# Performance work log

Measured on AMD Instinct MI355X. Metric: run time of the kernel, lower is better.

## Reference

```python
import jax, jax.numpy as jnp
import numpy as np

B, N, L, C, K = 2, 8192, 8192, 128, 8
RADIUS = 0.4

def _gather(t, idx):
    # t: [B,L,D], idx: [B,N,K] -> [B,N,K,D]
    b, n, k = idx.shape
    return jnp.take_along_axis(t, idx.reshape(b, n * k)[:, :, None], axis=1).reshape(b, n, k, t.shape[-1])

def _ln(x, g, b):
    m = x.mean(-1, keepdims=True)
    v = x.var(-1, keepdims=True)
    return (x - m) * jax.lax.rsqrt(v + 1e-5) * g + b

def setup_inputs() -> dict:
    key = jax.random.key(0)
    ks = jax.random.split(key, 16)
    F = 4 * C
    def w(k, i, o):
        return jax.random.normal(k, (i, o), jnp.float32) / np.sqrt(i).astype(np.float32)
    return {
        "q_xyz": jax.random.uniform(ks[0], (B, N, 3), jnp.float32),
        "q_feat": jax.random.normal(ks[1], (B, N, C), jnp.float32),
        "kv_xyz": jax.random.uniform(ks[2], (B, L, 3), jnp.float32),
        "kv_feat": jax.random.normal(ks[3], (B, L, C), jnp.float32),
        "kv_pad": jnp.zeros((B, L), bool),
        "pos_w1": w(ks[4], 3, C), "pos_b1": jnp.zeros((C,), jnp.float32),
        "pos_w2": w(ks[5], C, C), "pos_b2": jnp.zeros((C,), jnp.float32),
        "attn_w": w(ks[6], C, C), "attn_b": jnp.zeros((C,), jnp.float32),
        "lin_w": w(ks[7], C, C),
        "lin_src_w": w(ks[8], C, C),
        "lin_dst_w": w(ks[9], C, C),
        "ln1_g": jnp.ones((C,), jnp.float32), "ln1_b": jnp.zeros((C,), jnp.float32),
        "ffn_w1": w(ks[10], C, F), "ffn_b1": jnp.zeros((F,), jnp.float32),
        "ffn_w2": w(ks[11], F, C), "ffn_b2": jnp.zeros((C,), jnp.float32),
        "ln2_g": jnp.ones((C,), jnp.float32), "ln2_b": jnp.zeros((C,), jnp.float32),
    }

def reference(q_xyz, q_feat, kv_xyz, kv_feat, kv_pad,
              pos_w1, pos_b1, pos_w2, pos_b2, attn_w, attn_b,
              lin_w, lin_src_w, lin_dst_w, ln1_g, ln1_b,
              ffn_w1, ffn_b1, ffn_w2, ffn_b2, ln2_g, ln2_b):
    # --- radius graph: up to K nearest kv points within RADIUS per query ---
    d2 = jnp.sum((q_xyz[:, :, None, :] - kv_xyz[:, None, :, :]) ** 2, -1)  # [B,N,L]
    ok = (d2 <= RADIUS ** 2) & (~kv_pad)[:, None, :]
    neg_d2, idx = jax.lax.top_k(jnp.where(ok, -d2, -jnp.inf), K)  # [B,N,K]
    ev = jnp.isfinite(neg_d2)  # edge-valid mask [B,N,K]

    # --- PointTransformerConv (vector attention, per-edge) ---
    pos_j = _gather(kv_xyz, idx)                           # [B,N,K,3]
    rel = q_xyz[:, :, None, :] - pos_j                     # pos_i - pos_j
    # pos_nn: MLP([3,C,C], plain_last=False) => ReLU after each Linear
    delta = jax.nn.relu(jax.nn.relu(rel @ pos_w1 + pos_b1) @ pos_w2 + pos_b2)  # [B,N,K,C]
    a_src = _gather(kv_feat @ lin_src_w, idx)              # [B,N,K,C]
    a_dst = q_feat @ lin_dst_w                             # [B,N,C]
    x_j = _gather(kv_feat @ lin_w, idx)                    # [B,N,K,C]
    # attn_nn: MLP([C,C], plain_last=False) => Linear + ReLU
    alpha = jax.nn.relu((a_dst[:, :, None, :] - a_src + delta) @ attn_w + attn_b)
    # segment softmax over the K neighbors (invalid edges masked out)
    scores = jnp.where(ev[..., None], alpha, -jnp.inf)
    mx = jnp.max(scores, axis=2, keepdims=True)
    mx = jnp.where(jnp.isfinite(mx), mx, 0.0)
    e = jnp.where(ev[..., None], jnp.exp(scores - mx), 0.0)
    attn = e / jnp.maximum(e.sum(2, keepdims=True), 1e-12)
    agg = jnp.sum(attn * (x_j + delta), axis=2)            # [B,N,C]

    # --- residual + LN + FFN + LN (dropout = identity at eval) ---
    out = _ln(q_feat + agg, ln1_g, ln1_b)
    h = jax.nn.gelu(out @ ffn_w1 + ffn_b1, approximate=False) @ ffn_w2 + ffn_b2
    return _ln(out + h, ln2_g, ln2_b)
```

## Files before the change

### kernel.cpp

```cpp
#include <hip/hip_runtime.h>
#include <math.h>

#define NB 2
#define NQ 8192
#define NL 8192
#define NC 128
#define NKN 8
#define NF 512
#define MQ (NB*NQ)

typedef __attribute__((ext_vector_type(8))) short bf16x8;
typedef __attribute__((ext_vector_type(4))) float f32x4;

__device__ __forceinline__ unsigned short f2bf_u(float f){
    unsigned u = __float_as_uint(f);
    return (unsigned short)((u + 0x7FFFu + ((u>>16)&1u)) >> 16);
}
__device__ __forceinline__ float bf2f(unsigned short s){
    return __uint_as_float(((unsigned)s) << 16);
}


__device__ __forceinline__ int cell_coord(float x) {
    int c = (int)(x * 16.0f);
    return min(15, max(0, c));
}

__global__ __launch_bounds__(256) void grid_count_kernel(
    const float* __restrict__ kxyz, const unsigned char* __restrict__ pad,
    int* __restrict__ cnt)
{
    int t = blockIdx.x*256 + threadIdx.x;
    if (pad[t]) return;
    int bat = t >> 13;
    float x = kxyz[t*3+0], y = kxyz[t*3+1], z = kxyz[t*3+2];
    int cell = (cell_coord(z)*16 + cell_coord(y))*16 + cell_coord(x);
    atomicAdd(&cnt[bat*4096 + cell], 1);
}

__global__ __launch_bounds__(1024) void grid_scan_kernel(
    const int* __restrict__ cnt, int* __restrict__ cs)
{
    __shared__ int wsum[17];
    int t = threadIdx.x;
    int v[8]; int s = 0;
    #pragma unroll
    for (int k = 0; k < 8; ++k) { v[k] = s; s += cnt[t*8 + k]; }
    int lane = t & 63, w = t >> 6;
    int inc = s;
    #pragma unroll
    for (int d = 1; d < 64; d <<= 1) {
        int o = __shfl_up(inc, d);
        if (lane >= d) inc += o;
    }
    if (lane == 63) wsum[w] = inc;
    __syncthreads();
    if (t == 0) {
        int a = 0;
        for (int i = 0; i < 16; ++i) { int x = wsum[i]; wsum[i] = a; a += x; }
        wsum[16] = a;
    }
    __syncthreads();
    int base = wsum[w] + (inc - s);
    #pragma unroll
    for (int k = 0; k < 8; ++k) cs[t*8 + k] = base + v[k];
    if (t == 1023) cs[8192] = wsum[16];
}

__global__ __launch_bounds__(256) void grid_scatter_kernel(
    const float* __restrict__ kxyz, const unsigned char* __restrict__ pad,
    const int* __restrict__ cs, int* __restrict__ fill, float4* __restrict__ ro)
{
    int t = blockIdx.x*256 + threadIdx.x;
    if (pad[t]) return;
    int bat = t >> 13, i = t & 8191;
    float x = kxyz[t*3+0], y = kxyz[t*3+1], z = kxyz[t*3+2];
    int cell = bat*4096 + (cell_coord(z)*16 + cell_coord(y))*16 + cell_coord(x);
    int pos = cs[cell] + atomicAdd(&fill[cell], 1);
    ro[pos] = make_float4(x, y, z, __int_as_float(i));
}

__device__ __forceinline__ void insert8(float cd, int id, float dk[8], int ik[8]) {
    if (cd < dk[7]) {
        dk[7] = cd; ik[7] = id;
        #pragma unroll
        for (int r = 6; r >= 0; --r) {
            bool sw = dk[r+1] < dk[r];
            float td = dk[r]; int ti = ik[r];
            dk[r]   = sw ? dk[r+1] : dk[r];
            ik[r]   = sw ? ik[r+1] : ik[r];
            dk[r+1] = sw ? td : dk[r+1];
            ik[r+1] = sw ? ti : ik[r+1];
        }
    }
}

template<int W>
__device__ __forceinline__ void scan_block(int l, int cx, int cy, int cz,
    float qx, float qy, float qz, const int* __restrict__ CS,
    const float4* __restrict__ RO, float dk[8], int ik[8])
{
    const int D = 2*W + 1;
    int xs = max(0, cx - W), xe = min(15, cx + W);
    int nx = xe - xs + 1;
    for (int r = l; r < D*D; r += 8) {
        int dz = r / D - W, dy = r % D - W;
        int zz = cz + dz, yy = cy + dy;
        if ((unsigned)zz > 15u || (unsigned)yy > 15u) continue;
        int c0 = (zz*16 + yy)*16 + xs;
        int s = CS[c0], e = CS[c0 + nx];
        for (int p = s; p < e; ++p) {
            float4 v = RO[p];
            float dx = qx - v.x, dyv = qy - v.y, dzv = qz - v.z;
            float cd = dx*dx + dyv*dyv + dzv*dzv;
            insert8(cd, __float_as_int(v.w), dk, ik);
        }
    }
}

__device__ __forceinline__ void merge8(float dk[8], int ik[8]) {
    #pragma unroll
    for (int m = 1; m <= 4; m <<= 1) {
        float od[8]; int oi[8];
        #pragma unroll
        for (int r = 0; r < 8; ++r) {
            od[r] = __shfl_xor(dk[r], m);
            oi[r] = __shfl_xor(ik[r], m);
        }
        float nd[8]; int ni[8];
        #pragma unroll
        for (int r = 0; r < 8; ++r) {
            bool take = od[7-r] < dk[r];
            nd[r] = take ? od[7-r] : dk[r];
            ni[r] = take ? oi[7-r] : ik[r];
        }
        #pragma unroll
        for (int st = 4; st >= 1; st >>= 1) {
            #pragma unroll
            for (int r = 0; r < 8; ++r) {
                if ((r & st) == 0 && (r | st) < 8) {
                    int b = r | st;
                    bool sw = nd[b] < nd[r];
                    float td = nd[r]; int ti = ni[r];
                    nd[r] = sw ? nd[b] : nd[r];
                    ni[r] = sw ? ni[b] : ni[r];
                    nd[b] = sw ? td : nd[b];
                    ni[b] = sw ? ti : ni[b];
                }
            }
        }
        #pragma unroll
        for (int r = 0; r < 8; ++r) { dk[r] = nd[r]; ik[r] = ni[r]; }
    }
}

__global__ __launch_bounds__(256) void radius_grid_query_kernel(
    const float* __restrict__ qxyz, const int* __restrict__ cellstart,
    const float4* __restrict__ reorder, int* __restrict__ idxout)
{
    const int tid  = threadIdx.x;
    const int l    = tid & 7;
    const int qloc = tid >> 3;
    const int gq   = blockIdx.x*32 + qloc;
    const int bat  = gq >> 13;
    const float qx = qxyz[gq*3+0], qy = qxyz[gq*3+1], qz = qxyz[gq*3+2];
    const int cx = cell_coord(qx), cy = cell_coord(qy), cz = cell_coord(qz);
    const int* CS = cellstart + bat*4096;
    const float R2  = (float)(0.4*0.4);
    const float R2P = __uint_as_float(__float_as_uint(R2) + 1u);

    float dk[8]; int ik[8];
    #pragma unroll
    for (int r = 0; r < 8; ++r) { dk[r] = R2P; ik[r] = -1; }

    scan_block<2>(l, cx, cy, cz, qx, qy, qz, CS, reorder, dk, ik);
    merge8(dk, ik);
    bool done = dk[7] <= 0.015625f;

    if (!done) {
        #pragma unroll
        for (int r = 0; r < 8; ++r) { dk[r] = R2P; ik[r] = -1; }
        scan_block<4>(l, cx, cy, cz, qx, qy, qz, CS, reorder, dk, ik);
        merge8(dk, ik);
        done = dk[7] <= 0.0625f;
    }
    if (!done) {
        #pragma unroll
        for (int r = 0; r < 8; ++r) { dk[r] = R2P; ik[r] = -1; }
        scan_block<16>(l, cx, cy, cz, qx, qy, qz, CS, reorder, dk, ik);
        merge8(dk, ik);
    }

    if (l == 0) {
        int o[8];
        #pragma unroll
        for (int r = 0; r < 8; ++r) o[r] = (dk[r] <= R2) ? ik[r] : -1;
        int4 a = {o[0], o[1], o[2], o[3]};
        int4 b = {o[4], o[5], o[6], o[7]};
        *(int4*)&idxout[(size_t)gq*8 + 0] = a;
        *(int4*)&idxout[(size_t)gq*8 + 4] = b;
    }
}

__global__ __launch_bounds__(256) void prep_all_kernel(
    const float* __restrict__ posw2, const float* __restrict__ attnw,
    const float* __restrict__ lin_w, const float* __restrict__ lin_src_w,
    const float* __restrict__ lin_dst_w,
    const float* __restrict__ ffn_w1, const float* __restrict__ ffn_w2,
    unsigned short* __restrict__ imgb, int* __restrict__ zero_p)
{
    int t = blockIdx.x*256 + threadIdx.x;
    if (t < 16384) {
        int k = t >> 7, n = t & 127;
        imgb[(k >> 5)*4096 + n*32 + (k & 31)] = f2bf_u(posw2[t]);
    } else if (t < 32768) {
        int u = t - 16384;
        int k = u >> 7, n = u & 127;
        imgb[16384 + (k >> 5)*4096 + n*32 + (k & 31)] = f2bf_u(attnw[u]);
    } else if (t < 65536) {
        int u = t - 32768;
        int k = u >> 8, n = u & 255;
        float v = (n < 128) ? lin_w[k*128 + n] : lin_src_w[k*128 + (n-128)];
        imgb[32768 + ((k >> 5)*256 + n)*32 + (k & 31)] = f2bf_u(v);
    } else if (t < 81920) {
        int u = t - 65536;
        int k = u >> 7, n = u & 127;
        imgb[65536 + ((k >> 5)*128 + n)*32 + (k & 31)] = f2bf_u(lin_dst_w[u]);
    } else if (t < 147456) {
        int u = t - 81920;
        int k = u >> 9, n = u & 511;
        imgb[81920 + ((k >> 5)*512 + n)*32 + (k & 31)] = f2bf_u(ffn_w1[u]);
    } else if (t < 212992) {
        int u = t - 147456;
        int k = u >> 7, n = u & 127;
        imgb[147456 + ((k >> 5)*128 + n)*32 + (k & 31)] = f2bf_u(ffn_w2[u]);
    } else {
        zero_p[t - 212992] = 0;
    }
}

__global__ __launch_bounds__(256) void lin3_kernel(
    const float* __restrict__ kv_feat, const float* __restrict__ q_feat,
    const unsigned short* __restrict__ wvs, const unsigned short* __restrict__ wd,
    unsigned short* __restrict__ vs, float* __restrict__ adst)
{
    __shared__ unsigned short sA[64*32];
    __shared__ unsigned short sB[128*32];
    const int tid = threadIdx.x;
    const int w = tid >> 6, lane = tid & 63, l15 = lane & 15, quad = lane >> 4;
    const int row0 = blockIdx.x*64;
    const int y = blockIdx.y;
    const float* A = (y == 2) ? q_feat : kv_feat;
    const unsigned short* Bimg = (y == 2) ? wd : wvs;
    const int BNd = (y == 2) ? 128 : 256;
    const int col0 = (y == 2) ? 0 : y*128;

    f32x4 acc[8];
    #pragma unroll
    for (int t=0;t<8;t++){ acc[t][0]=0.f; acc[t][1]=0.f; acc[t][2]=0.f; acc[t][3]=0.f; }

    for (int kc = 0; kc < 4; ++kc) {
        __syncthreads();
        #pragma unroll
        for (int it = 0; it < 2; ++it) {
            int ix = it*256 + tid;
            int r = ix >> 3, kq = ix & 7;
            float4 a4 = *(const float4*)&A[(size_t)(row0+r)*NC + kc*32 + kq*4];
            ushort4 pk = { f2bf_u(a4.x), f2bf_u(a4.y), f2bf_u(a4.z), f2bf_u(a4.w) };
            *(ushort4*)&sA[r*32 + kq*4] = pk;
        }
        const int4* bsrc = (const int4*)(Bimg + ((size_t)kc*BNd + col0)*32);
        #pragma unroll
        for (int it = 0; it < 2; ++it) {
            int o = it*256 + tid;
            ((int4*)sB)[o] = bsrc[o];
        }
        __syncthreads();
        bf16x8 af = *(const bf16x8*)&sA[(w*16 + l15)*32 + quad*8];
        #pragma unroll
        for (int t = 0; t < 8; ++t) {
            bf16x8 bf = *(const bf16x8*)&sB[(16*t + l15)*32 + quad*8];
            acc[t] = __builtin_amdgcn_mfma_f32_16x16x32_bf16(af, bf, acc[t], 0, 0, 0);
        }
    }

    const int rowb = row0 + w*16 + quad*4;
    #pragma unroll
    for (int t = 0; t < 8; ++t) {
        int col = col0 + 16*t + l15;
        #pragma unroll
        for (int r = 0; r < 4; ++r) {
            if (y == 2) adst[(size_t)(rowb+r)*NC + col] = acc[t][r];
            else        vs[(size_t)(rowb+r)*256 + col] = f2bf_u(acc[t][r]);
        }
    }
}

__device__ inline float gelu_exact(float x) {
    return 0.5f*x*(1.0f + erff(x*0.7071067811865476f));
}

__global__ __launch_bounds__(256, 4) void ffn_fused_kernel(
    const float* __restrict__ in1,
    const unsigned short* __restrict__ wf1, const unsigned short* __restrict__ wf2,
    const float* __restrict__ b1v, const float* __restrict__ b2v,
    const float* __restrict__ g, const float* __restrict__ bb,
    float* __restrict__ out)
{
    __shared__ unsigned short sH[4*16*136];
    __shared__ float4 sS[16];
    __shared__ float4 sQ[16];
    const int tid = threadIdx.x;
    const int w = tid >> 6, lane = tid & 63, l15 = lane & 15, quad = lane >> 4;
    const int row0 = blockIdx.x*16;

    bf16x8 af[4];
    {
        const float* arow = in1 + (size_t)(row0 + l15)*NC;
        #pragma unroll
        for (int kk = 0; kk < 4; ++kk) {
            float4 a0 = *(const float4*)&arow[kk*32 + quad*8];
            float4 a1 = *(const float4*)&arow[kk*32 + quad*8 + 4];
            bf16x8 v;
            v[0]=(short)f2bf_u(a0.x); v[1]=(short)f2bf_u(a0.y);
            v[2]=(short)f2bf_u(a0.z); v[3]=(short)f2bf_u(a0.w);
            v[4]=(short)f2bf_u(a1.x); v[5]=(short)f2bf_u(a1.y);
            v[6]=(short)f2bf_u(a1.z); v[7]=(short)f2bf_u(a1.w);
            af[kk] = v;
        }
    }

    f32x4 acc1[8];
    #pragma unroll
    for (int t=0;t<8;t++){ acc1[t][0]=0.f; acc1[t][1]=0.f; acc1[t][2]=0.f; acc1[t][3]=0.f; }
    #pragma unroll
    for (int kk=0;kk<4;kk++){
        #pragma unroll
        for (int t=0;t<8;t++){
            int n = w*128 + 16*t + l15;
            bf16x8 bf = *(const bf16x8*)&wf1[((size_t)kk*512 + n)*32 + quad*8];
            acc1[t] = __builtin_amdgcn_mfma_f32_16x16x32_bf16(af[kk], bf, acc1[t], 0, 0, 0);
        }
    }

    {
        unsigned short* Hw = sH + w*(16*136);
        #pragma unroll
        for (int t=0;t<8;t++){
            float bv = b1v[w*128 + 16*t + l15];
            #pragma unroll
            for (int r=0;r<4;r++){
                float x = gelu_exact(acc1[t][r] + bv);
                Hw[(quad*4+r)*136 + 16*t + l15] = f2bf_u(x);
            }
        }
    }
    __syncthreads();

    f32x4 acc2[2];
    #pragma unroll
    for (int tt=0;tt<2;tt++){ acc2[tt][0]=0.f; acc2[tt][1]=0.f; acc2[tt][2]=0.f; acc2[tt][3]=0.f; }
    #pragma unroll
    for (int kkg=0;kkg<16;kkg++){
        const unsigned short* Ht = sH + (kkg>>2)*(16*136);
        bf16x8 a2 = *(const bf16x8*)&Ht[l15*136 + (kkg&3)*32 + quad*8];
        #pragma unroll
        for (int tt=0;tt<2;tt++){
            int col = (2*w+tt)*16 + l15;
            bf16x8 bf = *(const bf16x8*)&wf2[((size_t)kkg*128 + col)*32 + quad*8];
            acc2[tt] = __builtin_amdgcn_mfma_f32_16x16x32_bf16(a2, bf, acc2[tt], 0, 0, 0);
        }
    }

    float xv[2][4];
    float S0=0.f,S1=0.f,S2=0.f,S3=0.f;
    float Q0=0.f,Q1=0.f,Q2=0.f,Q3=0.f;
    #pragma unroll
    for (int tt=0;tt<2;tt++){
        int col = (2*w+tt)*16 + l15;
        float bv = b2v[col];
        #pragma unroll
        for (int r=0;r<4;r++){
            int row = row0 + quad*4 + r;
            float x = acc2[tt][r] + bv + in1[(size_t)row*NC + col];
            xv[tt][r] = x;
            if (r==0){ S0+=x; Q0+=x*x; } else if (r==1){ S1+=x; Q1+=x*x; }
            else if (r==2){ S2+=x; Q2+=x*x; } else { S3+=x; Q3+=x*x; }
        }
    }
    #pragma unroll
    for (int m=1;m<=8;m<<=1){
        S0 += __shfl_xor(S0,m); S1 += __shfl_xor(S1,m);
        S2 += __shfl_xor(S2,m); S3 += __shfl_xor(S3,m);
        Q0 += __shfl_xor(Q0,m); Q1 += __shfl_xor(Q1,m);
        Q2 += __shfl_xor(Q2,m); Q3 += __shfl_xor(Q3,m);
    }
    if (l15 == 0){
        sS[w*4 + quad] = make_float4(S0,S1,S2,S3);
        sQ[w*4 + quad] = make_float4(Q0,Q1,Q2,Q3);
    }
    __syncthreads();

    float4 St = sS[quad]; float4 Qt = sQ[quad];
    {
        float4 a = sS[4+quad],  b = sS[8+quad],  c = sS[12+quad];
        St.x += a.x+b.x+c.x; St.y += a.y+b.y+c.y; St.z += a.z+b.z+c.z; St.w += a.w+b.w+c.w;
        float4 d = sQ[4+quad], e = sQ[8+quad],  f = sQ[12+quad];
        Qt.x += d.x+e.x+f.x; Qt.y += d.y+e.y+f.y; Qt.z += d.z+e.z+f.z; Qt.w += d.w+e.w+f.w;
    }
    float mean[4], rstd[4];
    {
        float sv[4] = {St.x, St.y, St.z, St.w};
        float qv[4] = {Qt.x, Qt.y, Qt.z, Qt.w};
        #pragma unroll
        for (int r=0;r<4;r++){
            float m_ = sv[r]*(1.f/128.f);
            float v_ = qv[r]*(1.f/128.f) - m_*m_;
            mean[r] = m_;
            rstd[r] = rsqrtf(v_ + 1e-5f);
        }
    }
    #pragma unroll
    for (int tt=0;tt<2;tt++){
        int col = (2*w+tt)*16 + l15;
        float gv = g[col], bv = bb[col];
        #pragma unroll
        for (int r=0;r<4;r++){
            int row = row0 + quad*4 + r;
            out[(size_t)row*NC + col] = (xv[tt][r]-mean[r])*rstd[r]*gv + bv;
        }
    }
}

__global__ __launch_bounds__(256) void attn_mfma_kernel(
    const float* __restrict__ qxyz, const float* __restrict__ qfeat,
    const float* __restrict__ kxyz,
    const float* __restrict__ posw1, const float* __restrict__ posb1,
    const float* __restrict__ posb2, const float* __restrict__ attnb,
    const float* __restrict__ ln1g, const float* __restrict__ ln1b,
    const unsigned short* __restrict__ wimg1, const unsigned short* __restrict__ wimg2,
    const int* __restrict__ idx, const unsigned short* __restrict__ vs,
    const float* __restrict__ adst, float* __restrict__ out1)
{
    __shared__ unsigned short s_w[16384];
    __shared__ unsigned short s_V[4*16*136];
    __shared__ unsigned short s_T[4*16*136];
    __shared__ float s_w1[384];
    __shared__ float s_b1[128], s_b2[128], s_ab[128], s_g[128], s_bb[128];
    __shared__ int   s_j[64];

    const int tid  = threadIdx.x;
    const int w    = tid >> 6;
    const int lane = tid & 63;
    const int l15  = lane & 15;
    const int quad = lane >> 4;
    const int qbase = blockIdx.x*8 + w*2;
    const int bat  = (blockIdx.x*8) >> 13;

    if (tid < 128) {
        s_b1[tid] = posb1[tid]; s_b2[tid] = posb2[tid];
        s_ab[tid] = attnb[tid]; s_g[tid] = ln1g[tid]; s_bb[tid] = ln1b[tid];
    } else {
        int i = tid - 128;
        s_w1[i] = posw1[i]; s_w1[128+i] = posw1[128+i]; s_w1[256+i] = posw1[256+i];
    }
    if (tid < 64) s_j[tid] = idx[(size_t)blockIdx.x*64 + tid];
    #pragma unroll
    for (int r = 0; r < 8; ++r)
        ((int4*)s_w)[r*256 + tid] = ((const int4*)wimg1)[r*256 + tid];
    __syncthreads();

    #pragma unroll
    for (int i = 0; i < 4; ++i) {
        int ix = lane + i*64;
        int el = ix >> 4, c16 = ix & 15;
        int j = s_j[w*16 + el];
        int jc = j < 0 ? 0 : j;
        const int4* rp = (const int4*)(vs + ((size_t)(bat*NL + jc))*256);
        int dst = (w*16 + el)*136 + c16*8;
        *(int4*)&s_V[dst] = rp[c16];
        *(int4*)&s_T[dst] = rp[16 + c16];
    }

    bf16x8 h1f[4];
    {
        int e  = w*16 + l15;
        int qh = qbase + (l15 >> 3);
        int j  = s_j[e];
        int jc = j < 0 ? 0 : j;
        const float* kp = kxyz + ((size_t)(bat*NL + jc))*3;
        float rx = qxyz[qh*3+0]-kp[0], ry = qxyz[qh*3+1]-kp[1], rz = qxyz[qh*3+2]-kp[2];
        #pragma unroll
        for (int kk=0;kk<4;kk++){
            #pragma unroll
            for (int jj=0;jj<8;jj++){
                int c = kk*32 + quad*8 + jj;
                float h = s_b1[c] + rx*s_w1[c] + ry*s_w1[128+c] + rz*s_w1[256+c];
                h = fmaxf(h, 0.f);
                h1f[kk][jj] = (short)f2bf_u(h);
            }
        }
    }

    f32x4 acc[8];
    #pragma unroll
    for (int t=0;t<8;t++){ acc[t][0]=0.f; acc[t][1]=0.f; acc[t][2]=0.f; acc[t][3]=0.f; }
    #pragma unroll
    for (int kk=0;kk<4;kk++){
        #pragma unroll
        for (int t=0;t<8;t++){
            bf16x8 wf = *(const bf16x8*)&s_w[kk*4096 + (16*t + l15)*32 + quad*8];
            acc[t] = __builtin_amdgcn_mfma_f32_16x16x32_bf16(h1f[kk], wf, acc[t], 0, 0, 0);
        }
    }

    f32x4 dreg[8];
    #pragma unroll
    for (int t=0;t<8;t++){
        float b2v = s_b2[16*t + l15];
        #pragma unroll
        for (int r=0;r<4;r++) dreg[t][r] = fmaxf(acc[t][r] + b2v, 0.f);
    }

    int jr[4]; bool val[4];
    #pragma unroll
    for (int r=0;r<4;r++){
        int j = s_j[w*16 + quad*4 + r];
        val[r] = (j >= 0); jr[r] = j < 0 ? 0 : j;
    }
    const int qt = qbase + (quad >> 1);
    float ad[8];
    #pragma unroll
    for (int t=0;t<8;t++) ad[t] = adst[(size_t)qt*NC + 16*t + l15];

    __syncthreads();

    #pragma unroll
    for (int r = 0; r < 8; ++r)
        ((int4*)s_w)[r*256 + tid] = ((const int4*)wimg2)[r*256 + tid];

    {
        unsigned short* st = s_T + w*16*136;
        #pragma unroll
        for (int t=0;t<8;t++){
            #pragma unroll
            for (int r=0;r<4;r++){
                int o = (quad*4 + r)*136 + 16*t + l15;
                float sv = bf2f(st[o]);
                st[o] = f2bf_u(ad[t] - sv + dreg[t][r]);
            }
        }
    }
    __syncthreads();

    f32x4 acc2[8];
    #pragma unroll
    for (int t=0;t<8;t++){ acc2[t][0]=0.f; acc2[t][1]=0.f; acc2[t][2]=0.f; acc2[t][3]=0.f; }
    {
        const unsigned short* st = s_T + w*16*136;
        #pragma unroll
        for (int kk=0;kk<4;kk++){
            bf16x8 tf = *(const bf16x8*)&st[l15*136 + kk*32 + quad*8];
            #pragma unroll
            for (int t=0;t<8;t++){
                bf16x8 wf = *(const bf16x8*)&s_w[kk*4096 + (16*t + l15)*32 + quad*8];
                acc2[t] = __builtin_amdgcn_mfma_f32_16x16x32_bf16(tf, wf, acc2[t], 0, 0, 0);
            }
        }
    }

    float ex[8][4]; float dnm[8];
    #pragma unroll
    for (int t=0;t<8;t++){
        float ab = s_ab[16*t + l15];
        float s0 = val[0] ? fmaxf(acc2[t][0] + ab, 0.f) : -INFINITY;
        float s1 = val[1] ? fmaxf(acc2[t][1] + ab, 0.f) : -INFINITY;
        float s2 = val[2] ? fmaxf(acc2[t][2] + ab, 0.f) : -INFINITY;
        float s3 = val[3] ? fmaxf(acc2[t][3] + ab, 0.f) : -INFINITY;
        float mx = fmaxf(fmaxf(s0,s1), fmaxf(s2,s3));
        mx = fmaxf(mx, __shfl_xor(mx, 16));
        if (mx < -1e37f) mx = 0.f;
        ex[t][0] = __expf(s0 - mx);
        ex[t][1] = __expf(s1 - mx);
        ex[t][2] = __expf(s2 - mx);
        ex[t][3] = __expf(s3 - mx);
        float sm = ex[t][0]+ex[t][1]+ex[t][2]+ex[t][3];
        sm += __shfl_xor(sm, 16);
        dnm[t] = fmaxf(sm, 1e-12f);
    }

    float part[8];
    #pragma unroll
    for (int t=0;t<8;t++){
        float p = 0.f;
        #pragma unroll
        for (int r=0;r<4;r++){
            float vv = bf2f(s_V[(w*16 + quad*4 + r)*136 + 16*t + l15]);
            p += ex[t][r] * (vv + dreg[t][r]);
        }
        p += __shfl_xor(p, 16);
        part[t] = p / dnm[t];
    }

    float xln[8];
    float S = 0.f;
    #pragma unroll
    for (int t=0;t<8;t++){
        xln[t] = qfeat[(size_t)qt*NC + 16*t + l15] + part[t];
        S += xln[t];
    }
    #pragma unroll
    for (int m=1;m<=8;m<<=1) S += __shfl_xor(S, m);
    float mean = S * (1.f/128.f);
    float V = 0.f;
    #pragma unroll
    for (int t=0;t<8;t++){ float d = xln[t]-mean; V += d*d; }
    #pragma unroll
    for (int m=1;m<=8;m<<=1) V += __shfl_xor(V, m);
    float rstd = rsqrtf(V*(1.f/128.f) + 1e-5f);

    if ((quad & 1) == 0){
        #pragma unroll
        for (int t=0;t<8;t++){
            int c = 16*t + l15;
            out1[(size_t)qt*NC + c] = (xln[t]-mean)*rstd*s_g[c] + s_bb[c];
        }
    }
}

extern "C" void kernel_launch(void* const* d_in, const int* in_sizes, int n_in,
                              void* d_out, int out_size, void* d_ws, size_t ws_size,
                              hipStream_t stream)
{
    (void)in_sizes; (void)n_in; (void)out_size; (void)ws_size;
    const float* q_xyz   = (const float*)d_in[0];
    const float* q_feat  = (const float*)d_in[1];
    const float* kv_xyz  = (const float*)d_in[2];
    const float* kv_feat = (const float*)d_in[3];
    const unsigned char* kv_pad = (const unsigned char*)d_in[4];
    const float* pos_w1  = (const float*)d_in[5];
    const float* pos_b1  = (const float*)d_in[6];
    const float* pos_w2  = (const float*)d_in[7];
    const float* pos_b2  = (const float*)d_in[8];
    const float* attn_w  = (const float*)d_in[9];
    const float* attn_b  = (const float*)d_in[10];
    const float* lin_w   = (const float*)d_in[11];
    const float* lin_src_w = (const float*)d_in[12];
    const float* lin_dst_w = (const float*)d_in[13];
    const float* ln1_g   = (const float*)d_in[14];
    const float* ln1_b   = (const float*)d_in[15];
    const float* ffn_w1  = (const float*)d_in[16];
    const float* ffn_b1  = (const float*)d_in[17];
    const float* ffn_w2  = (const float*)d_in[18];
    const float* ffn_b2  = (const float*)d_in[19];
    const float* ln2_g   = (const float*)d_in[20];
    const float* ln2_b   = (const float*)d_in[21];

    float* ws    = (float*)d_ws;
    int*   idx   = (int*)d_ws;
    unsigned short* vs = (unsigned short*)(ws + 131072);
    float* adst  = ws + 131072 + 2*2097152;
    float* out1  = adst + 2097152;
    float* Hreg  = out1 + 2097152;

    float4* reorder  = (float4*)Hreg;
    int* cellcnt   = (int*)(reorder + 16384);
    int* cellfill  = cellcnt + 8192;
    int* cellstart = cellfill + 8192;

    unsigned short* imgb  = (unsigned short*)((char*)Hreg + (1u << 20));
    unsigned short* wimg1 = imgb;
    unsigned short* wimg2 = imgb + 16384;
    unsigned short* wvs   = imgb + 32768;
    unsigned short* wd    = imgb + 65536;
    unsigned short* wf1   = imgb + 81920;
    unsigned short* wf2   = imgb + 147456;

    prep_all_kernel<<<dim3(896), dim3(256), 0, stream>>>(
        pos_w2, attn_w, lin_w, lin_src_w, lin_dst_w, ffn_w1, ffn_w2, imgb, cellcnt);

    grid_count_kernel<<<dim3(64), dim3(256), 0, stream>>>(kv_xyz, kv_pad, cellcnt);
    grid_scan_kernel<<<dim3(1), dim3(1024), 0, stream>>>(cellcnt, cellstart);
    grid_scatter_kernel<<<dim3(64), dim3(256), 0, stream>>>(kv_xyz, kv_pad, cellstart, cellfill, reorder);
    radius_grid_query_kernel<<<dim3(MQ/32), dim3(256), 0, stream>>>(q_xyz, cellstart, reorder, idx);

    lin3_kernel<<<dim3(MQ/64, 3), dim3(256), 0, stream>>>(kv_feat, q_feat, wvs, wd, vs, adst);

    attn_mfma_kernel<<<dim3(MQ/8), dim3(256), 0, stream>>>(
        q_xyz, q_feat, kv_xyz,
        pos_w1, pos_b1, pos_b2, attn_b, ln1_g, ln1_b,
        wimg1, wimg2, idx, vs, adst, out1);

    ffn_fused_kernel<<<dim3(MQ/16), dim3(256), 0, stream>>>(
        out1, wf1, wf2, ffn_b1, ffn_b2, ln2_g, ln2_b, (float*)d_out);
}
```

Baseline: 219.7 us.

## Read attention MLP weights from global instead of LDS to raise occupancy

Drops the 32KB shared-memory staging of the two bf16 weight images in the attention kernel. MFMA B-fragments are now loaded straight from global memory, relying on the L1/L2 caches. Removing the staging also removes two block-wide barriers, since the remaining LDS buffers are only used within each wave. It adds a launch-bounds occupancy hint and fuses the softmax and aggregation loops to lower register pressure. The risk is higher global/L2 traffic and latency on weight fetches inside the MFMA loops.

Measured after the change: 223.6 us. No clear change (+1.8%).

```diff
diff --git a/kernel.cpp b/kernel.cpp
--- a/kernel.cpp
+++ b/kernel.cpp
@@ -432,7 +432,7 @@
     }
 }
 
-__global__ __launch_bounds__(256) void attn_mfma_kernel(
+__global__ __launch_bounds__(256, 4) void attn_mfma_kernel(
     const float* __restrict__ qxyz, const float* __restrict__ qfeat,
     const float* __restrict__ kxyz,
     const float* __restrict__ posw1, const float* __restrict__ posb1,
@@ -442,7 +442,6 @@
     const int* __restrict__ idx, const unsigned short* __restrict__ vs,
     const float* __restrict__ adst, float* __restrict__ out1)
 {
-    __shared__ unsigned short s_w[16384];
     __shared__ unsigned short s_V[4*16*136];
     __shared__ unsigned short s_T[4*16*136];
     __shared__ float s_w1[384];
@@ -465,9 +464,6 @@
         s_w1[i] = posw1[i]; s_w1[128+i] = posw1[128+i]; s_w1[256+i] = posw1[256+i];
     }
     if (tid < 64) s_j[tid] = idx[(size_t)blockIdx.x*64 + tid];
-    #pragma unroll
-    for (int r = 0; r < 8; ++r)
-        ((int4*)s_w)[r*256 + tid] = ((const int4*)wimg1)[r*256 + tid];
     __syncthreads();
 
     #pragma unroll
@@ -509,7 +505,7 @@
     for (int kk=0;kk<4;kk++){
         #pragma unroll
         for (int t=0;t<8;t++){
-            bf16x8 wf = *(const bf16x8*)&s_w[kk*4096 + (16*t + l15)*32 + quad*8];
+            bf16x8 wf = *(const bf16x8*)&wimg1[kk*4096 + (16*t + l15)*32 + quad*8];
             acc[t] = __builtin_amdgcn_mfma_f32_16x16x32_bf16(h1f[kk], wf, acc[t], 0, 0, 0);
         }
     }
@@ -522,22 +518,16 @@
         for (int r=0;r<4;r++) dreg[t][r] = fmaxf(acc[t][r] + b2v, 0.f);
     }
 
-    int jr[4]; bool val[4];
+    bool val[4];
     #pragma unroll
     for (int r=0;r<4;r++){
         int j = s_j[w*16 + quad*4 + r];
-        val[r] = (j >= 0); jr[r] = j < 0 ? 0 : j;
+        val[r] = (j >= 0);
     }
     const int qt = qbase + (quad >> 1);
     float ad[8];
     #pragma unroll
     for (int t=0;t<8;t++) ad[t] = adst[(size_t)qt*NC + 16*t + l15];
-
-    __syncthreads();
-
-    #pragma unroll
-    for (int r = 0; r < 8; ++r)
-        ((int4*)s_w)[r*256 + tid] = ((const int4*)wimg2)[r*256 + tid];
 
     {
         unsigned short* st = s_T + w*16*136;
@@ -551,7 +541,6 @@
             }
         }
     }
-    __syncthreads();
 
     f32x4 acc2[8];
     #pragma unroll
@@ -563,13 +552,13 @@
             bf16x8 tf = *(const bf16x8*)&st[l15*136 + kk*32 + quad*8];
             #pragma unroll
             for (int t=0;t<8;t++){
-                bf16x8 wf = *(const bf16x8*)&s_w[kk*4096 + (16*t + l15)*32 + quad*8];
+                bf16x8 wf = *(const bf16x8*)&wimg2[kk*4096 + (16*t + l15)*32 + quad*8];
                 acc2[t] = __builtin_amdgcn_mfma_f32_16x16x32_bf16(tf, wf, acc2[t], 0, 0, 0);
             }
         }
     }
 
-    float ex[8][4]; float dnm[8];
+    float part[8];
     #pragma unroll
     for (int t=0;t<8;t++){
         float ab = s_ab[16*t + l15];
@@ -580,26 +569,20 @@
         float mx = fmaxf(fmaxf(s0,s1), fmaxf(s2,s3));
         mx = fmaxf(mx, __shfl_xor(mx, 16));
         if (mx < -1e37f) mx = 0.f;
-        ex[t][0] = __expf(s0 - mx);
-        ex[t][1] = __expf(s1 - mx);
-        ex[t][2] = __expf(s2 - mx);
-        ex[t][3] = __expf(s3 - mx);
-        float sm = ex[t][0]+ex[t][1]+ex[t][2]+ex[t][3];
+        float e0 = __expf(s0 - mx);
+        float e1 = __expf(s1 - mx);
+        float e2 = __expf(s2 - mx);
+        float e3 = __expf(s3 - mx);
+        float sm = e0+e1+e2+e3;
         sm += __shfl_xor(sm, 16);
-        dnm[t] = fmaxf(sm, 1e-12f);
-    }
-
-    float part[8];
-    #pragma unroll
-    for (int t=0;t<8;t++){
+        float dnm = fmaxf(sm, 1e-12f);
         float p = 0.f;
-        #pragma unroll
-        for (int r=0;r<4;r++){
-            float vv = bf2f(s_V[(w*16 + quad*4 + r)*136 + 16*t + l15]);
-            p += ex[t][r] * (vv + dreg[t][r]);
-        }
+        p += e0 * (bf2f(s_V[(w*16 + quad*4 + 0)*136 + 16*t + l15]) + dreg[t][0]);
+        p += e1 * (bf2f(s_V[(w*16 + quad*4 + 1)*136 + 16*t + l15]) + dreg[t][1]);
+        p += e2 * (bf2f(s_V[(w*16 + quad*4 + 2)*136 + 16*t + l15]) + dreg[t][2]);
+        p += e3 * (bf2f(s_V[(w*16 + quad*4 + 3)*136 + 16*t + l15]) + dreg[t][3]);
         p += __shfl_xor(p, 16);
-        part[t] = p / dnm[t];
+        part[t] = p / dnm;
     }
 
     float xln[8];
```

## Double rows per block in FFN and attention kernels to amortize weight loads

Applied to the files above, without the earlier changes.

The FFN kernel now handles 32 rows per block instead of 16. Each block computes two 16-row tiles, so every weight fragment loaded from global memory feeds two MFMAs. The attention kernel grows to 512 threads covering 16 queries, so the shared weight images are staged once for twice the work. The cost is more registers and shared memory per block, which may lower occupancy, and the grids have half as many blocks.

Measured after the change: 216.6 us. No clear change (-1.4%).

```diff
diff --git a/kernel.cpp b/kernel.cpp
--- a/kernel.cpp
+++ b/kernel.cpp
@@ -300,139 +300,169 @@
     return 0.5f*x*(1.0f + erff(x*0.7071067811865476f));
 }
 
-__global__ __launch_bounds__(256, 4) void ffn_fused_kernel(
+__global__ __launch_bounds__(256) void ffn_fused_kernel(
     const float* __restrict__ in1,
     const unsigned short* __restrict__ wf1, const unsigned short* __restrict__ wf2,
     const float* __restrict__ b1v, const float* __restrict__ b2v,
     const float* __restrict__ g, const float* __restrict__ bb,
     float* __restrict__ out)
 {
-    __shared__ unsigned short sH[4*16*136];
-    __shared__ float4 sS[16];
-    __shared__ float4 sQ[16];
+    __shared__ unsigned short sH[8*16*136];
+    __shared__ float4 sS[2][16];
+    __shared__ float4 sQ[2][16];
     const int tid = threadIdx.x;
     const int w = tid >> 6, lane = tid & 63, l15 = lane & 15, quad = lane >> 4;
-    const int row0 = blockIdx.x*16;
-
-    bf16x8 af[4];
+    const int row0 = blockIdx.x*32;
+
+    bf16x8 af0[4], af1[4];
     {
-        const float* arow = in1 + (size_t)(row0 + l15)*NC;
+        const float* arow0 = in1 + (size_t)(row0 + l15)*NC;
+        const float* arow1 = in1 + (size_t)(row0 + 16 + l15)*NC;
         #pragma unroll
         for (int kk = 0; kk < 4; ++kk) {
-            float4 a0 = *(const float4*)&arow[kk*32 + quad*8];
-            float4 a1 = *(const float4*)&arow[kk*32 + quad*8 + 4];
+            float4 a0 = *(const float4*)&arow0[kk*32 + quad*8];
+            float4 a1 = *(const float4*)&arow0[kk*32 + quad*8 + 4];
             bf16x8 v;
             v[0]=(short)f2bf_u(a0.x); v[1]=(short)f2bf_u(a0.y);
             v[2]=(short)f2bf_u(a0.z); v[3]=(short)f2bf_u(a0.w);
             v[4]=(short)f2bf_u(a1.x); v[5]=(short)f2bf_u(a1.y);
             v[6]=(short)f2bf_u(a1.z); v[7]=(short)f2bf_u(a1.w);
-            af[kk] = v;
-        }
-    }
-
-    f32x4 acc1[8];
-    #pragma unroll
-    for (int t=0;t<8;t++){ acc1[t][0]=0.f; acc1[t][1]=0.f; acc1[t][2]=0.f; acc1[t][3]=0.f; }
+            af0[kk] = v;
+            float4 b0 = *(const float4*)&arow1[kk*32 + quad*8];
+            float4 b1 = *(const float4*)&arow1[kk*32 + quad*8 + 4];
+            bf16x8 u;
+            u[0]=(short)f2bf_u(b0.x); u[1]=(short)f2bf_u(b0.y);
+            u[2]=(short)f2bf_u(b0.z); u[3]=(short)f2bf_u(b0.w);
+            u[4]=(short)f2bf_u(b1.x); u[5]=(short)f2bf_u(b1.y);
+            u[6]=(short)f2bf_u(b1.z); u[7]=(short)f2bf_u(b1.w);
+            af1[kk] = u;
+        }
+    }
+
+    f32x4 acc1a[8], acc1b[8];
+    #pragma unroll
+    for (int t=0;t<8;t++){
+        acc1a[t][0]=0.f; acc1a[t][1]=0.f; acc1a[t][2]=0.f; acc1a[t][3]=0.f;
+        acc1b[t][0]=0.f; acc1b[t][1]=0.f; acc1b[t][2]=0.f; acc1b[t][3]=0.f;
+    }
     #pragma unroll
     for (int kk=0;kk<4;kk++){
         #pragma unroll
         for (int t=0;t<8;t++){
             int n = w*128 + 16*t + l15;
             bf16x8 bf = *(const bf16x8*)&wf1[((size_t)kk*512 + n)*32 + quad*8];
-            acc1[t] = __builtin_amdgcn_mfma_f32_16x16x32_bf16(af[kk], bf, acc1[t], 0, 0, 0);
+            acc1a[t] = __builtin_amdgcn_mfma_f32_16x16x32_bf16(af0[kk], bf, acc1a[t], 0, 0, 0);
+            acc1b[t] = __builtin_amdgcn_mfma_f32_16x16x32_bf16(af1[kk], bf, acc1b[t], 0, 0, 0);
         }
     }
 
     {
-        unsigned short* Hw = sH + w*(16*136);
+        unsigned short* Hw0 = sH + (w)*(16*136);
+        unsigned short* Hw1 = sH + (4 + w)*(16*136);
         #pragma unroll
         for (int t=0;t<8;t++){
             float bv = b1v[w*128 + 16*t + l15];
             #pragma unroll
             for (int r=0;r<4;r++){
-                float x = gelu_exact(acc1[t][r] + bv);
-                Hw[(quad*4+r)*136 + 16*t + l15] = f2bf_u(x);
+                float x0 = gelu_exact(acc1a[t][r] + bv);
+                Hw0[(quad*4+r)*136 + 16*t + l15] = f2bf_u(x0);
+                float x1 = gelu_exact(acc1b[t][r] + bv);
+                Hw1[(quad*4+r)*136 + 16*t + l15] = f2bf_u(x1);
             }
         }
     }
     __syncthreads();
 
-    f32x4 acc2[2];
-    #pragma unroll
-    for (int tt=0;tt<2;tt++){ acc2[tt][0]=0.f; acc2[tt][1]=0.f; acc2[tt][2]=0.f; acc2[tt][3]=0.f; }
+    f32x4 acc2a[2], acc2b[2];
+    #pragma unroll
+    for (int tt=0;tt<2;tt++){
+        acc2a[tt][0]=0.f; acc2a[tt][1]=0.f; acc2a[tt][2]=0.f; acc2a[tt][3]=0.f;
+        acc2b[tt][0]=0.f; acc2b[tt][1]=0.f; acc2b[tt][2]=0.f; acc2b[tt][3]=0.f;
+    }
     #pragma unroll
     for (int kkg=0;kkg<16;kkg++){
-        const unsigned short* Ht = sH + (kkg>>2)*(16*136);
-        bf16x8 a2 = *(const bf16x8*)&Ht[l15*136 + (kkg&3)*32 + quad*8];
+        const unsigned short* Ht0 = sH + (kkg>>2)*(16*136);
+        const unsigned short* Ht1 = sH + (4 + (kkg>>2))*(16*136);
+        bf16x8 a2a = *(const bf16x8*)&Ht0[l15*136 + (kkg&3)*32 + quad*8];
+        bf16x8 a2b = *(const bf16x8*)&Ht1[l15*136 + (kkg&3)*32 + quad*8];
         #pragma unroll
         for (int tt=0;tt<2;tt++){
             int col = (2*w+tt)*16 + l15;
             bf16x8 bf = *(const bf16x8*)&wf2[((size_t)kkg*128 + col)*32 + quad*8];
-            acc2[tt] = __builtin_amdgcn_mfma_f32_16x16x32_bf16(a2, bf, acc2[tt], 0, 0, 0);
-        }
-    }
-
-    float xv[2][4];
-    float S0=0.f,S1=0.f,S2=0.f,S3=0.f;
-    float Q0=0.f,Q1=0.f,Q2=0.f,Q3=0.f;
-    #pragma unroll
-    for (int tt=0;tt<2;tt++){
-        int col = (2*w+tt)*16 + l15;
-        float bv = b2v[col];
-        #pragma unroll
-        for (int r=0;r<4;r++){
-            int row = row0 + quad*4 + r;
-            float x = acc2[tt][r] + bv + in1[(size_t)row*NC + col];
-            xv[tt][r] = x;
-            if (r==0){ S0+=x; Q0+=x*x; } else if (r==1){ S1+=x; Q1+=x*x; }
-            else if (r==2){ S2+=x; Q2+=x*x; } else { S3+=x; Q3+=x*x; }
-        }
-    }
-    #pragma unroll
-    for (int m=1;m<=8;m<<=1){
-        S0 += __shfl_xor(S0,m); S1 += __shfl_xor(S1,m);
-        S2 += __shfl_xor(S2,m); S3 += __shfl_xor(S3,m);
-        Q0 += __shfl_xor(Q0,m); Q1 += __shfl_xor(Q1,m);
-        Q2 += __shfl_xor(Q2,m); Q3 += __shfl_xor(Q3,m);
-    }
-    if (l15 == 0){
-        sS[w*4 + quad] = make_float4(S0,S1,S2,S3);
-        sQ[w*4 + quad] = make_float4(Q0,Q1,Q2,Q3);
+            acc2a[tt] = __builtin_amdgcn_mfma_f32_16x16x32_bf16(a2a, bf, acc2a[tt], 0, 0, 0);
+            acc2b[tt] = __builtin_amdgcn_mfma_f32_16x16x32_bf16(a2b, bf, acc2b[tt], 0, 0, 0);
+        }
+    }
+
+    float xv[2][2][4];
+    float Ssum[2][4], Qsum[2][4];
+    #pragma unroll
+    for (int tile=0; tile<2; ++tile){
+        #pragma unroll
+        for (int r=0;r<4;r++){ Ssum[tile][r]=0.f; Qsum[tile][r]=0.f; }
+        #pragma unroll
+        for (int tt=0;tt<2;tt++){
+            int col = (2*w+tt)*16 + l15;
+            float bv = b2v[col];
+            #pragma unroll
+            for (int r=0;r<4;r++){
+                int row = row0 + tile*16 + quad*4 + r;
+                float a = (tile==0) ? acc2a[tt][r] : acc2b[tt][r];
+                float x = a + bv + in1[(size_t)row*NC + col];
+                xv[tile][tt][r] = x;
+                Ssum[tile][r] += x; Qsum[tile][r] += x*x;
+            }
+        }
+        #pragma unroll
+        for (int m=1;m<=8;m<<=1){
+            #pragma unroll
+            for (int r=0;r<4;r++){
+                Ssum[tile][r] += __shfl_xor(Ssum[tile][r], m);
+                Qsum[tile][r] += __shfl_xor(Qsum[tile][r], m);
+            }
+        }
+        if (l15 == 0){
+            sS[tile][w*4 + quad] = make_float4(Ssum[tile][0],Ssum[tile][1],Ssum[tile][2],Ssum[tile][3]);
+            sQ[tile][w*4 + quad] = make_float4(Qsum[tile][0],Qsum[tile][1],Qsum[tile][2],Qsum[tile][3]);
+        }
     }
     __syncthreads();
 
-    float4 St = sS[quad]; float4 Qt = sQ[quad];
-    {
-        float4 a = sS[4+quad],  b = sS[8+quad],  c = sS[12+quad];
-        St.x += a.x+b.x+c.x; St.y += a.y+b.y+c.y; St.z += a.z+b.z+c.z; St.w += a.w+b.w+c.w;
-        float4 d = sQ[4+quad], e = sQ[8+quad],  f = sQ[12+quad];
-        Qt.x += d.x+e.x+f.x; Qt.y += d.y+e.y+f.y; Qt.z += d.z+e.z+f.z; Qt.w += d.w+e.w+f.w;
-    }
-    float mean[4], rstd[4];
-    {
-        float sv[4] = {St.x, St.y, St.z, St.w};
-        float qv[4] = {Qt.x, Qt.y, Qt.z, Qt.w};
-        #pragma unroll
-        for (int r=0;r<4;r++){
-            float m_ = sv[r]*(1.f/128.f);
-            float v_ = qv[r]*(1.f/128.f) - m_*m_;
-            mean[r] = m_;
-            rstd[r] = rsqrtf(v_ + 1e-5f);
-        }
-    }
-    #pragma unroll
-    for (int tt=0;tt<2;tt++){
-        int col = (2*w+tt)*16 + l15;
-        float gv = g[col], bv = bb[col];
-        #pragma unroll
-        for (int r=0;r<4;r++){
-            int row = row0 + quad*4 + r;
-            out[(size_t)row*NC + col] = (xv[tt][r]-mean[r])*rstd[r]*gv + bv;
-        }
-    }
-}
-
-__global__ __launch_bounds__(256) void attn_mfma_kernel(
+    #pragma unroll
+    for (int tile=0; tile<2; ++tile){
+        float4 St = sS[tile][quad]; float4 Qt = sQ[tile][quad];
+        {
+            float4 a = sS[tile][4+quad],  b = sS[tile][8+quad],  c = sS[tile][12+quad];
+            St.x += a.x+b.x+c.x; St.y += a.y+b.y+c.y; St.z += a.z+b.z+c.z; St.w += a.w+b.w+c.w;
+            float4 d = sQ[tile][4+quad], e = sQ[tile][8+quad],  f = sQ[tile][12+quad];
+            Qt.x += d.x+e.x+f.x; Qt.y += d.y+e.y+f.y; Qt.z += d.z+e.z+f.z; Qt.w += d.w+e.w+f.w;
+        }
+        float mean[4], rstd[4];
+        {
+            float sv[4] = {St.x, St.y, St.z, St.w};
+            float qv[4] = {Qt.x, Qt.y, Qt.z, Qt.w};
+            #pragma unroll
+            for (int r=0;r<4;r++){
+                float m_ = sv[r]*(1.f/128.f);
+                float v_ = qv[r]*(1.f/128.f) - m_*m_;
+                mean[r] = m_;
+                rstd[r] = rsqrtf(v_ + 1e-5f);
+            }
+        }
+        #pragma unroll
+        for (int tt=0;tt<2;tt++){
+            int col = (2*w+tt)*16 + l15;
+            float gv = g[col], bv = bb[col];
+            #pragma unroll
+            for (int r=0;r<4;r++){
+                int row = row0 + tile*16 + quad*4 + r;
+                out[(size_t)row*NC + col] = (xv[tile][tt][r]-mean[r])*rstd[r]*gv + bv;
+            }
+        }
+    }
+}
+
+__global__ __launch_bounds__(512) void attn_mfma_kernel(
     const float* __restrict__ qxyz, const float* __restrict__ qfeat,
     const float* __restrict__ kxyz,
     const float* __restrict__ posw1, const float* __restrict__ posb1,
@@ -443,31 +473,31 @@
     const float* __restrict__ adst, float* __restrict__ out1)
 {
     __shared__ unsigned short s_w[16384];
-    __shared__ unsigned short s_V[4*16*136];
-    __shared__ unsigned short s_T[4*16*136];
+    __shared__ unsigned short s_V[8*16*136];
+    __shared__ unsigned short s_T[8*16*136];
     __shared__ float s_w1[384];
     __shared__ float s_b1[128], s_b2[128], s_ab[128], s_g[128], s_bb[128];
-    __shared__ int   s_j[64];
+    __shared__ int   s_j[128];
 
     const int tid  = threadIdx.x;
     const int w    = tid >> 6;
     const int lane = tid & 63;
     const int l15  = lane & 15;
     const int quad = lane >> 4;
-    const int qbase = blockIdx.x*8 + w*2;
-    const int bat  = (blockIdx.x*8) >> 13;
+    const int qbase = blockIdx.x*16 + w*2;
+    const int bat  = (blockIdx.x*16) >> 13;
 
     if (tid < 128) {
         s_b1[tid] = posb1[tid]; s_b2[tid] = posb2[tid];
         s_ab[tid] = attnb[tid]; s_g[tid] = ln1g[tid]; s_bb[tid] = ln1b[tid];
-    } else {
+    } else if (tid < 256) {
         int i = tid - 128;
         s_w1[i] = posw1[i]; s_w1[128+i] = posw1[128+i]; s_w1[256+i] = posw1[256+i];
     }
-    if (tid < 64) s_j[tid] = idx[(size_t)blockIdx.x*64 + tid];
-    #pragma unroll
-    for (int r = 0; r < 8; ++r)
-        ((int4*)s_w)[r*256 + tid] = ((const int4*)wimg1)[r*256 + tid];
+    if (tid < 128) s_j[tid] = idx[(size_t)blockIdx.x*128 + tid];
+    #pragma unroll
+    for (int r = 0; r < 4; ++r)
+        ((int4*)s_w)[r*512 + tid] = ((const int4*)wimg1)[r*512 + tid];
     __syncthreads();
 
     #pragma unroll
@@ -522,11 +552,11 @@
         for (int r=0;r<4;r++) dreg[t][r] = fmaxf(acc[t][r] + b2v, 0.f);
     }
 
-    int jr[4]; bool val[4];
+    bool val[4];
     #pragma unroll
     for (int r=0;r<4;r++){
         int j = s_j[w*16 + quad*4 + r];
-        val[r] = (j >= 0); jr[r] = j < 0 ? 0 : j;
+        val[r] = (j >= 0);
     }
     const int qt = qbase + (quad >> 1);
     float ad[8];
@@ -536,8 +566,8 @@
     __syncthreads();
 
     #pragma unroll
-    for (int r = 0; r < 8; ++r)
-        ((int4*)s_w)[r*256 + tid] = ((const int4*)wimg2)[r*256 + tid];
+    for (int r = 0; r < 4; ++r)
+        ((int4*)s_w)[r*512 + tid] = ((const int4*)wimg2)[r*512 + tid];
 
     {
         unsigned short* st = s_T + w*16*136;
@@ -686,11 +716,11 @@
 
     lin3_kernel<<<dim3(MQ/64, 3), dim3(256), 0, stream>>>(kv_feat, q_feat, wvs, wd, vs, adst);
 
-    attn_mfma_kernel<<<dim3(MQ/8), dim3(256), 0, stream>>>(
+    attn_mfma_kernel<<<dim3(MQ/16), dim3(512), 0, stream>>>(
         q_xyz, q_feat, kv_xyz,
         pos_w1, pos_b1, pos_b2, attn_b, ln1_g, ln1_b,
         wimg1, wimg2, idx, vs, adst, out1);
 
-    ffn_fused_kernel<<<dim3(MQ/16), dim3(256), 0, stream>>>(
+    ffn_fused_kernel<<<dim3(MQ/32), dim3(256), 0, stream>>>(
         out1, wf1, wf2, ffn_b1, ffn_b2, ln2_g, ln2_b, (float*)d_out);
 }
```
